# Optimization experiments

Hardware: AMD Instinct MI355X
Metric: run time of the kernel (lower is better)

Reference implementation:

```python
import jax, jax.numpy as jnp
from jax import lax
import numpy as np

# (cin, cout, kernel, pad) for the 18 convs (funs 1,3,5,6,7,9,10,11,13..17,19..23)
CONVS = [(3,32,3,0),(32,64,3,0),(64,128,3,1),(128,64,1,0),(64,128,3,1),
         (128,256,3,1),(256,128,1,0),(128,256,3,0),(256,512,3,1),(512,256,1,0),
         (256,512,3,1),(512,256,1,0),(256,512,3,0),(512,256,3,1),(256,128,1,0),
         (128,64,3,1),(64,32,1,0),(32,6,3,1)]
# maxpool(2,2) after conv index (1-based) -> pool padding (torch pads with -inf, floor mode)
POOL_AFTER = {1: 1, 2: 1, 5: 0, 8: 1, 13: 1}
GT = (0.567, 0.469, 0.206, 0.53)  # hardcoded ground-truth box (cx, cy, w, h), normalized


def _backbone(x, ws, bs):
    for i, (w, b) in enumerate(zip(ws, bs), 1):
        pad = CONVS[i - 1][3]
        x = lax.conv_general_dilated(
            x, w, (1, 1), [(pad, pad), (pad, pad)],
            dimension_numbers=("NCHW", "OIHW", "NCHW")) + b[None, :, None, None]
        if i in POOL_AFTER:
            p = POOL_AFTER[i]
            x = lax.reduce_window(
                x, -jnp.inf, lax.max, (1, 1, 2, 2), (1, 1, 2, 2),
                [(0, 0), (0, 0), (p, p), (p, p)])
    return x


def _head(x):
    # torch: x.transpose(1,3) on [B,6,H,W] -> [B,W,H,6]; j indexes W, k indexes H
    xt = jnp.transpose(x, (0, 3, 2, 1))
    B, W, H, _ = xt.shape
    j = jnp.arange(W, dtype=xt.dtype)[None, :, None]  # [1,W,1]
    k = jnp.arange(H, dtype=xt.dtype)[None, None, :]  # [1,1,H]
    px = (j + xt[..., 2]) / W
    py = (k + xt[..., 3]) / H
    pw = jnp.exp(xt[..., 4]) / W
    ph = jnp.exp(xt[..., 5]) / H
    # center-format IoU against the single gt box (detached mask, as in torch via float())
    iw = jnp.clip(jnp.minimum(px + pw * 0.5, GT[0] + GT[2] * 0.5)
                  - jnp.maximum(px - pw * 0.5, GT[0] - GT[2] * 0.5), 0.0)
    ih = jnp.clip(jnp.minimum(py + ph * 0.5, GT[1] + GT[3] * 0.5)
                  - jnp.maximum(py - ph * 0.5, GT[1] - GT[3] * 0.5), 0.0)
    inter = iw * ih
    iou = inter / (pw * ph + GT[2] * GT[3] - inter)
    iou = lax.stop_gradient(iou)
    tx = GT[0] * W - j          # [1,W,1]
    ty = GT[1] * H - k          # [1,1,H]
    tw = np.log(GT[2] * W).astype(np.float32)
    th = np.log(GT[3] * H).astype(np.float32)
    l1 = (jnp.abs(tx - xt[..., 2]) + jnp.abs(ty - xt[..., 3])
          + jnp.abs(tw - xt[..., 4]) + jnp.abs(th - xt[..., 5]))
    loss = jnp.sum(jnp.where(iou > 0.5, l1, 0.0)).reshape(1)
    return xt, loss


def setup_inputs() -> dict:
    key = jax.random.key(0)
    keys = jax.random.split(key, 1 + 2 * len(CONVS))
    d = {"x": jax.random.normal(keys[0], (16, 3, 416, 416), jnp.float32)}
    for i, (cin, cout, ks, _) in enumerate(CONVS, 1):
        fan_in = cin * ks * ks
        d[f"w{i}"] = jax.random.normal(keys[2 * i - 1], (cout, cin, ks, ks), jnp.float32) / np.sqrt(fan_in)
        d[f"b{i}"] = jax.random.normal(keys[2 * i], (cout,), jnp.float32) * 0.01
    return d


def reference(x, w1, b1, w2, b2, w3, b3, w4, b4, w5, b5, w6, b6, w7, b7, w8, b8,
              w9, b9, w10, b10, w11, b11, w12, b12, w13, b13, w14, b14, w15, b15,
              w16, b16, w17, b17, w18, b18):
    ws = [w1, w2, w3, w4, w5, w6, w7, w8, w9, w10, w11, w12, w13, w14, w15, w16, w17, w18]
    bs = [b1, b2, b3, b4, b5, b6, b7, b8, b9, b10, b11, b12, b13, b14, b15, b16, b17, b18]
    feat = _backbone(x, ws, bs)
    xt, loss = _head(feat)
    return (xt, loss)
```

## Files before the change

### kernel.cpp

```cpp
#include <hip/hip_runtime.h>
#include <math.h>

typedef short v8s __attribute__((ext_vector_type(8)));
typedef float v4f __attribute__((ext_vector_type(4)));

template<int K, int COT, bool POOL>
__global__ __launch_bounds__(256) void conv_fused(
    const float* __restrict__ in, const float* __restrict__ wgt,
    const float* __restrict__ bias, float* __restrict__ out,
    int B, int Cin, int Hin, int Win,
    int Hc, int Wc, int Hout, int Wout,
    int Cout, int cpad, int ppad)
{
    constexpr int NPY = POOL ? 2 : 1;
    constexpr int PS  = K + NPY - 1;
    const int spatial = Hout * Wout;
    const int idx = blockIdx.x * blockDim.x + threadIdx.x;
    const int total = B * spatial;
    if (idx >= total) return;
    const int b  = idx / spatial;
    const int sp = idx - b * spatial;
    const int oy = sp / Wout;
    const int ox = sp - oy * Wout;
    const int co0 = blockIdx.y * COT;

    const int cy0 = POOL ? (2 * oy - ppad) : oy;
    const int cx0 = POOL ? (2 * ox - ppad) : ox;
    const int iy0 = cy0 - cpad;
    const int ix0 = cx0 - cpad;

    bool my[PS], mx[PS];
#pragma unroll
    for (int i = 0; i < PS; i++) {
        my[i] = (unsigned)(iy0 + i) < (unsigned)Hin;
        mx[i] = (unsigned)(ix0 + i) < (unsigned)Win;
    }

    float acc[COT][NPY * NPY];
#pragma unroll
    for (int c = 0; c < COT; c++)
#pragma unroll
        for (int p = 0; p < NPY * NPY; p++) acc[c][p] = 0.f;

    const long inBase = (long)b * Cin * Hin * Win;
    const long wBase  = (long)co0 * Cin * K * K;

    for (int ci = 0; ci < Cin; ci++) {
        const float* ip = in + inBase + (long)ci * Hin * Win;
        float patch[PS][PS];
#pragma unroll
        for (int py = 0; py < PS; py++) {
#pragma unroll
            for (int px = 0; px < PS; px++) {
                float v = 0.f;
                if (my[py] && mx[px]) v = ip[(iy0 + py) * Win + (ix0 + px)];
                patch[py][px] = v;
            }
        }
        const float* wp = wgt + wBase + (long)ci * K * K;
#pragma unroll
        for (int c = 0; c < COT; c++) {
#pragma unroll
            for (int kh = 0; kh < K; kh++)
#pragma unroll
            for (int kw = 0; kw < K; kw++) {
                const float wv = wp[(long)c * Cin * K * K + kh * K + kw];
#pragma unroll
                for (int dy = 0; dy < NPY; dy++)
#pragma unroll
                for (int dx = 0; dx < NPY; dx++)
                    acc[c][dy * NPY + dx] = fmaf(wv, patch[dy + kh][dx + kw],
                                                 acc[c][dy * NPY + dx]);
            }
        }
    }

#pragma unroll
    for (int c = 0; c < COT; c++) {
        float v;
        if (POOL) {
            v = -INFINITY;
#pragma unroll
            for (int dy = 0; dy < NPY; dy++)
#pragma unroll
            for (int dx = 0; dx < NPY; dx++) {
                const int cy = cy0 + dy, cx = cx0 + dx;
                if ((unsigned)cy < (unsigned)Hc && (unsigned)cx < (unsigned)Wc)
                    v = fmaxf(v, acc[c][dy * NPY + dx]);
            }
        } else {
            v = acc[c][0];
        }
        v += bias[co0 + c];
        out[((long)(b * Cout + co0 + c)) * spatial + sp] = v;
    }
}

__device__ __forceinline__ unsigned short f2bf_rne(float x) {
    unsigned u = __float_as_uint(x);
    return (unsigned short)((u + 0x7fffu + ((u >> 16) & 1u)) >> 16);
}
__device__ __forceinline__ float bf2f(unsigned short h) {
    return __uint_as_float(((unsigned)h) << 16);
}

__global__ __launch_bounds__(256) void prepack(
    const float* __restrict__ w, unsigned short* __restrict__ hi,
    unsigned short* __restrict__ lo, int cout, int kdim, int nkb)
{
    int t = blockIdx.x * 256 + threadIdx.x;
    if (t >= cout * kdim) return;
    int co = t / kdim, k = t - co * kdim;
    int cb = co >> 4, m = co & 15, kb = k >> 5, kk = k & 31;
    int lane = ((kk >> 3) << 4) | m, j = kk & 7;
    long dst = ((long)(cb * nkb + kb) << 9) + lane * 8 + j;
    float x = w[t];
    unsigned short h = f2bf_rne(x);
    hi[dst] = h;
    lo[dst] = f2bf_rne(x - bf2f(h));
}

template<int MT, int KS, bool SPLIT>
__global__ __launch_bounds__(256) void conv_mfma(
    const float* __restrict__ in, const unsigned short* __restrict__ whi,
    const unsigned short* __restrict__ wlo, const float* __restrict__ bias,
    float* __restrict__ out, int Cin, int Hin, int Win, int Hc, int Wc,
    int Cout, int pad, int b0, int nb, int nkbTot, int nkbPer, int Mpad)
{
    const int HW = Hc * Wc;
    const int M = nb * HW;
    const int tid = threadIdx.x;
    const int lane = tid & 63;
    const int wv = tid >> 6;
    const int spBase = blockIdx.x * 64;
    const int HWin = Hin * Win;
    const int kb0 = SPLIT ? blockIdx.z * nkbPer : 0;
    const int kb1 = SPLIT ? kb0 + nkbPer : nkbTot;

    __shared__ unsigned short P[2][5120];

    const int spoL = lane >> 2;
    int kkc[2];
    kkc[0] = (tid & 3) + 4 * wv;
    kkc[1] = kkc[0] + 16;

    const float* sptr[4];
    int soy[4], sox[4], soff[4];
    bool sval[4];
#pragma unroll
    for (int j = 0; j < 4; ++j) {
        int spo = spoL + 16 * j;
        int sp = spBase + spo;
        sval[j] = sp < M;
        int q = sval[j] ? sp : 0;
        int b = q / HW; int r = q - b * HW;
        soy[j] = r / Wc; sox[j] = r - soy[j] * Wc;
        soff[j] = soy[j] * Win + sox[j];
        sptr[j] = in + (size_t)(b0 + b) * Cin * HWin;
    }

    int ci[2], r9[2], dh[2], dw[2], koff[2];
#pragma unroll
    for (int m = 0; m < 2; ++m) {
        int k = kb0 * 32 + kkc[m];
        if (KS == 3) {
            ci[m] = k / 9; r9[m] = k - 9 * ci[m];
            int d3 = (r9[m] >= 3) + (r9[m] >= 6);
            dh[m] = d3 - pad; dw[m] = r9[m] - 3 * d3 - pad;
        } else { ci[m] = k; dh[m] = 0; dw[m] = 0; }
        koff[m] = ci[m] * HWin + dh[m] * Win + dw[m];
    }

    float rv[8];
#define STAGE()                                                                \
    {                                                                          \
        _Pragma("unroll")                                                      \
        for (int m = 0; m < 2; ++m)                                            \
        _Pragma("unroll")                                                      \
        for (int j = 0; j < 4; ++j) {                                          \
            int iy = soy[j] + dh[m], ix = sox[j] + dw[m];                      \
            bool ok = sval[j] && ((unsigned)iy < (unsigned)Hin) &&             \
                      ((unsigned)ix < (unsigned)Win);                          \
            rv[m * 4 + j] = ok ? sptr[j][koff[m] + soff[j]] : 0.f;             \
        }                                                                      \
    }
#define ADVANCE()                                                              \
    {                                                                          \
        _Pragma("unroll")                                                      \
        for (int m = 0; m < 2; ++m) {                                          \
            if (KS == 3) {                                                     \
                r9[m] += 5; int c = r9[m] >= 9; r9[m] -= c ? 9 : 0;            \
                ci[m] += 3 + c;                                                \
                int d3 = (r9[m] >= 3) + (r9[m] >= 6);                          \
                dh[m] = d3 - pad; dw[m] = r9[m] - 3 * d3 - pad;                \
                koff[m] = ci[m] * HWin + dh[m] * Win + dw[m];                  \
            } else { koff[m] += 32 * HWin; }                                   \
        }                                                                      \
    }

    STAGE();

    const int g0 = blockIdx.y * (MT * 4) + wv * MT;
    const unsigned short* whp[MT];
    const unsigned short* wlp[MT];
#pragma unroll
    for (int mt = 0; mt < MT; ++mt) {
        size_t base = (((size_t)(g0 + mt) * nkbTot + kb0) << 9) + lane * 8;
        whp[mt] = whi + base; wlp[mt] = wlo + base;
    }

    v4f acc[MT][4];
    {
        v4f z = {0.f, 0.f, 0.f, 0.f};
#pragma unroll
        for (int mt = 0; mt < MT; ++mt)
#pragma unroll
            for (int nt = 0; nt < 4; ++nt) acc[mt][nt] = z;
    }

    for (int kb = kb0; kb < kb1; ++kb) {
        unsigned short* Ph = P[kb & 1];
#pragma unroll
        for (int m = 0; m < 2; ++m)
#pragma unroll
        for (int j = 0; j < 4; ++j) {
            float v = rv[m * 4 + j];
            unsigned vb = __float_as_uint(v);
            float res = v - __uint_as_float(vb & 0xffff0000u);
            int a = (spoL + 16 * j) * 40 + kkc[m];
            Ph[a] = (unsigned short)(vb >> 16);
            Ph[2560 + a] = (unsigned short)(__float_as_uint(res) >> 16);
        }
        __syncthreads();

        v8s wh[MT], wl[MT];
#pragma unroll
        for (int mt = 0; mt < MT; ++mt) {
            wh[mt] = *(const v8s*)whp[mt];
            wl[mt] = *(const v8s*)wlp[mt];
            whp[mt] += 512; wlp[mt] += 512;
        }

        if (kb + 1 < kb1) { ADVANCE(); STAGE(); }

#pragma unroll
        for (int nt = 0; nt < 4; ++nt) {
            int ro = (nt * 16 + (lane & 15)) * 40 + (lane >> 4) * 8;
            v8s ph = *(const v8s*)(Ph + ro);
            v8s pl = *(const v8s*)(Ph + 2560 + ro);
#pragma unroll
            for (int mt = 0; mt < MT; ++mt) {
                acc[mt][nt] = __builtin_amdgcn_mfma_f32_16x16x32_bf16(wh[mt], ph, acc[mt][nt], 0, 0, 0);
                acc[mt][nt] = __builtin_amdgcn_mfma_f32_16x16x32_bf16(wh[mt], pl, acc[mt][nt], 0, 0, 0);
                acc[mt][nt] = __builtin_amdgcn_mfma_f32_16x16x32_bf16(wl[mt], ph, acc[mt][nt], 0, 0, 0);
            }
        }
    }
#undef STAGE
#undef ADVANCE

    const int qrow = (lane >> 4) * 4;
    if (SPLIT) {
        float* pz = out + (size_t)blockIdx.z * Cout * Mpad;
#pragma unroll
        for (int mt = 0; mt < MT; ++mt) {
            int co = (g0 + mt) * 16 + qrow;
#pragma unroll
            for (int nt = 0; nt < 4; ++nt) {
                int sp = spBase + nt * 16 + (lane & 15);
                if (sp < M) {
#pragma unroll
                    for (int r = 0; r < 4; ++r)
                        pz[(size_t)(co + r) * Mpad + sp] = acc[mt][nt][r];
                }
            }
        }
    } else {
#pragma unroll
        for (int mt = 0; mt < MT; ++mt) {
            int co = (g0 + mt) * 16 + qrow;
            float bsv[4];
#pragma unroll
            for (int r = 0; r < 4; ++r) bsv[r] = bias[co + r];
#pragma unroll
            for (int nt = 0; nt < 4; ++nt) {
                int sp = spBase + nt * 16 + (lane & 15);
                if (sp < M) {
                    int b = sp / HW, rsp = sp - b * HW;
                    float* op = out + ((size_t)(b * Cout + co)) * HW + rsp;
#pragma unroll
                    for (int r = 0; r < 4; ++r)
                        op[(size_t)r * HW] = acc[mt][nt][r] + bsv[r];
                }
            }
        }
    }
}

__global__ __launch_bounds__(256) void sk_reduce(
    const float* __restrict__ part, const float* __restrict__ bias,
    float* __restrict__ out, int Cout, int HW, int M, int Mpad, int SK)
{
    int t = blockIdx.x * 256 + threadIdx.x;
    if (t >= Cout * M) return;
    int co = t / M, m = t - co * M;
    float s = bias[co];
    for (int k = 0; k < SK; ++k)
        s += part[((size_t)k * Cout + co) * Mpad + m];
    int b = m / HW, rsp = m - b * HW;
    out[((size_t)(b * Cout + co)) * HW + rsp] = s;
}

__global__ __launch_bounds__(256) void maxpool_k(
    const float* __restrict__ in, float* __restrict__ out,
    int C, int Hc, int Wc, int Hp, int Wp, int p, int total)
{
    int t = blockIdx.x * 256 + threadIdx.x;
    if (t >= total) return;
    int wp2 = Hp * Wp;
    int bc = t / wp2; int r = t - bc * wp2;
    int y = r / Wp, xx = r - y * Wp;
    int y0 = 2 * y - p, x0 = 2 * xx - p;
    const float* ip = in + (size_t)bc * Hc * Wc;
    float v = -INFINITY;
#pragma unroll
    for (int dy = 0; dy < 2; ++dy)
#pragma unroll
    for (int dx = 0; dx < 2; ++dx) {
        int yy = y0 + dy, xc = x0 + dx;
        if ((unsigned)yy < (unsigned)Hc && (unsigned)xc < (unsigned)Wc)
            v = fmaxf(v, ip[yy * Wc + xc]);
    }
    out[t] = v;
}

__global__ __launch_bounds__(1024) void head_kernel(
    const float* __restrict__ x, float* __restrict__ out, int B)
{
    const int W = 13, H = 13;
    const float gx = 0.567f, gy = 0.469f, gw = 0.206f, gh = 0.53f;
    const int tid = threadIdx.x;
    const int total = B * W * H;
    float lsum = 0.f;
    for (int i = tid; i < total; i += blockDim.x) {
        const int b = i / (W * H);
        const int r = i - b * W * H;
        const int j = r / H;
        const int k = r - j * H;
        float v[6];
#pragma unroll
        for (int c = 0; c < 6; c++) {
            v[c] = x[((b * 6 + c) * H + k) * W + j];
            out[((b * W + j) * H + k) * 6 + c] = v[c];
        }
        const float px = (j + v[2]) / (float)W;
        const float py = (k + v[3]) / (float)H;
        const float pw = expf(v[4]) / (float)W;
        const float ph = expf(v[5]) / (float)H;
        float iw = fminf(px + pw * 0.5f, gx + gw * 0.5f)
                 - fmaxf(px - pw * 0.5f, gx - gw * 0.5f);
        iw = fmaxf(iw, 0.f);
        float ih = fminf(py + ph * 0.5f, gy + gh * 0.5f)
                 - fmaxf(py - ph * 0.5f, gy - gh * 0.5f);
        ih = fmaxf(ih, 0.f);
        const float inter = iw * ih;
        const float iou = inter / (pw * ph + gw * gh - inter);
        const float tx = gx * W - (float)j;
        const float ty = gy * H - (float)k;
        const float tw = logf(gw * W);
        const float th = logf(gh * H);
        const float l1 = fabsf(tx - v[2]) + fabsf(ty - v[3])
                       + fabsf(tw - v[4]) + fabsf(th - v[5]);
        if (iou > 0.5f) lsum += l1;
    }
    __shared__ float red[1024];
    red[tid] = lsum;
    __syncthreads();
    for (int s = blockDim.x / 2; s > 0; s >>= 1) {
        if (tid < s) red[tid] += red[tid + s];
        __syncthreads();
    }
    if (tid == 0) out[total * 6] = red[0];
}

extern "C" void kernel_launch(void* const* d_in, const int* in_sizes, int n_in,
                              void* d_out, int out_size, void* d_ws, size_t ws_size,
                              hipStream_t stream)
{
    (void)in_sizes; (void)n_in; (void)out_size;
    const float* x = (const float*)d_in[0];
    const int B = 16;
    const size_t MB = 1024 * 1024;
    char* ws = (char*)d_ws;
    float* bufA = (float*)ws;
    float* bufB = (float*)(ws + 90 * MB);
    unsigned short* WHI = (unsigned short*)(ws + 135 * MB);
    unsigned short* WLO = (unsigned short*)(ws + 147 * MB);
    char* TEMP = ws + 159 * MB;
    const bool gemmOK = ws_size >= 159 * MB;
    const size_t tempAvail = ws_size > 159 * MB ? ws_size - 159 * MB : 0;

    static const struct { int cin, cout, ks, cpad, pool, ppad; } L[18] = {
        {3,  32, 3, 0, 1, 1}, {32, 64, 3, 0, 1, 1}, {64, 128, 3, 1, 0, 0},
        {128, 64, 1, 0, 0, 0}, {64, 128, 3, 1, 1, 0}, {128, 256, 3, 1, 0, 0},
        {256, 128, 1, 0, 0, 0}, {128, 256, 3, 0, 1, 1}, {256, 512, 3, 1, 0, 0},
        {512, 256, 1, 0, 0, 0}, {256, 512, 3, 1, 0, 0}, {512, 256, 1, 0, 0, 0},
        {256, 512, 3, 0, 1, 1}, {512, 256, 3, 1, 0, 0}, {256, 128, 1, 0, 0, 0},
        {128, 64, 3, 1, 0, 0}, {64, 32, 1, 0, 0, 0}, {32, 6, 3, 1, 0, 0}
    };

    if (gemmOK) {
        size_t off = 0;
        for (int i = 1; i <= 15; ++i) {
            int kdim = L[i].cin * L[i].ks * L[i].ks;
            int n = L[i].cout * kdim;
            prepack<<<(n + 255) / 256, 256, 0, stream>>>(
                (const float*)d_in[2 * i + 1], WHI + off, WLO + off,
                L[i].cout, kdim, kdim / 32);
            off += (size_t)n;
        }
    }

    const float* cur = x;
    int Hin = 416, Win = 416;
    size_t woff = 0;

    for (int i = 0; i < 18; ++i) {
        const auto& l = L[i];
        const int Hc = Hin + 2 * l.cpad - l.ks + 1;
        const int Wc = Win + 2 * l.cpad - l.ks + 1;
        const int Hout = l.pool ? (Hc + 2 * l.ppad - 2) / 2 + 1 : Hc;
        const int Wout = l.pool ? (Wc + 2 * l.ppad - 2) / 2 + 1 : Wc;
        float* dst = (i % 2 == 0) ? bufA : bufB;
        const float* w  = (const float*)d_in[2 * i + 1];
        const float* bb = (const float*)d_in[2 * i + 2];
        const int kdim = l.cin * l.ks * l.ks;
        const int nkb = kdim / 32;

        int nb = 16;
        if (l.pool) {
            size_t perImg = (size_t)l.cout * Hc * Wc * 4;
            while (nb && perImg * (size_t)nb > tempAvail) nb >>= 1;
        }
        const bool useG = gemmOK && i >= 1 && i <= 15 && (!l.pool || nb >= 1);

        if (useG) {
            for (int b0 = 0; b0 < B; b0 += nb) {
                const int M = nb * Hc * Wc;
                const int gx = (M + 63) / 64;
                int MTv = (l.cout >= 256 && (long)gx * (l.cout / 256) >= 512) ? 4
                        : (l.cout >= 128 && (long)gx * (l.cout / 128) >= 512) ? 2 : 1;
                int gy = l.cout / (MTv * 64);
                int SK = 1;
                if (!l.pool && (long)gx * gy < 512) {
                    if (nkb % 4 == 0 && (size_t)4 * l.cout * gx * 64 * 4 <= tempAvail) SK = 4;
                    else if (nkb % 2 == 0 && (size_t)2 * l.cout * gx * 64 * 4 <= tempAvail) SK = 2;
                }
                const int nkbPer = nkb / SK;
                const int Mpad = gx * 64;
                float* gout = l.pool ? (float*)TEMP
                            : (SK > 1 ? (float*)TEMP : dst);
                dim3 gr(gx, gy, SK);
#define GL(MTC, KSC, SPL)                                                      \
                conv_mfma<MTC, KSC, SPL><<<gr, 256, 0, stream>>>(              \
                    cur, WHI + woff, WLO + woff, bb, gout, l.cin, Hin, Win,    \
                    Hc, Wc, l.cout, l.cpad, b0, nb, nkb, nkbPer, Mpad)
#define G2(MTC, KSC) do { if (SK > 1) GL(MTC, KSC, true); else GL(MTC, KSC, false); } while (0)
                if (MTv == 4)      { if (l.ks == 3) G2(4, 3); else G2(4, 1); }
                else if (MTv == 2) { if (l.ks == 3) G2(2, 3); else G2(2, 1); }
                else               { if (l.ks == 3) G2(1, 3); else G2(1, 1); }
#undef G2
#undef GL
                if (SK > 1) {
                    int tot = l.cout * M;
                    sk_reduce<<<(tot + 255) / 256, 256, 0, stream>>>(
                        (const float*)TEMP, bb, dst, l.cout, Hc * Wc, M, Mpad, SK);
                }
                if (l.pool) {
                    int total = nb * l.cout * Hout * Wout;
                    maxpool_k<<<(total + 255) / 256, 256, 0, stream>>>(
                        (const float*)TEMP,
                        dst + (size_t)b0 * l.cout * Hout * Wout,
                        l.cout, Hc, Wc, Hout, Wout, l.ppad, total);
                }
            }
        } else {
            const int spatial = Hout * Wout;
#define FLAUNCH(KK, CC, PP)                                                    \
            conv_fused<KK, CC, PP><<<dim3((B * spatial + 255) / 256,           \
                                          l.cout / CC), 256, 0, stream>>>(     \
                cur, w, bb, dst, B, l.cin, Hin, Win, Hc, Wc, Hout, Wout,       \
                l.cout, l.cpad, l.ppad)
            if (l.pool)                           FLAUNCH(3, 4, true);
            else if (l.ks == 3 && l.cout == 6)    FLAUNCH(3, 6, false);
            else if (l.ks == 3)                   FLAUNCH(3, 8, false);
            else                                  FLAUNCH(1, 8, false);
#undef FLAUNCH
        }

        if (i >= 1 && i <= 15) woff += (size_t)l.cout * kdim;
        cur = dst;
        Hin = Hout;
        Win = Wout;
    }

    head_kernel<<<1, 1024, 0, stream>>>(cur, (float*)d_out, B);
}
```

Baseline: 1.544 ms.

## Store activations with a zero halo ring to drop conv bounds checks

Activation buffers get a one-pixel zero border around every plane. A small ring_zero kernel writes the borders, and the MFMA im2col loads, the direct convs, split-K reduce and maxpool all index into the padded layout, so the per-element bounds checks in the gather are gone. The first layer also switches to a COT=8 fused conv with a swapped grid so channel groups sharing the same input tile run together. The cost is extra ring-zeroing launches, larger workspace offsets and padded strides that may misalign accesses. Padded buffers that are read with pad=0 must never depend on the ring being zero.

```diff
diff --git a/kernel.cpp b/kernel.cpp
--- a/kernel.cpp
+++ b/kernel.cpp
@@ -4,25 +4,27 @@
 typedef short v8s __attribute__((ext_vector_type(8)));
 typedef float v4f __attribute__((ext_vector_type(4)));
 
-template<int K, int COT, bool POOL>
+template<int K, int COT, bool POOL, bool MASK, bool SWAP>
 __global__ __launch_bounds__(256) void conv_fused(
     const float* __restrict__ in, const float* __restrict__ wgt,
     const float* __restrict__ bias, float* __restrict__ out,
     int B, int Cin, int Hin, int Win,
     int Hc, int Wc, int Hout, int Wout,
-    int Cout, int cpad, int ppad)
+    int Cout, int cpad, int ppad,
+    int inPS, int inRS, int inOfs, int outPS, int outRS, int outOfs)
 {
     constexpr int NPY = POOL ? 2 : 1;
     constexpr int PS  = K + NPY - 1;
     const int spatial = Hout * Wout;
-    const int idx = blockIdx.x * blockDim.x + threadIdx.x;
+    const int idx = (SWAP ? blockIdx.y : blockIdx.x) * blockDim.x + threadIdx.x;
+    const int cog = SWAP ? blockIdx.x : blockIdx.y;
     const int total = B * spatial;
     if (idx >= total) return;
     const int b  = idx / spatial;
     const int sp = idx - b * spatial;
     const int oy = sp / Wout;
     const int ox = sp - oy * Wout;
-    const int co0 = blockIdx.y * COT;
+    const int co0 = cog * COT;
 
     const int cy0 = POOL ? (2 * oy - ppad) : oy;
     const int cx0 = POOL ? (2 * ox - ppad) : ox;
@@ -32,8 +34,8 @@
     bool my[PS], mx[PS];
 #pragma unroll
     for (int i = 0; i < PS; i++) {
-        my[i] = (unsigned)(iy0 + i) < (unsigned)Hin;
-        mx[i] = (unsigned)(ix0 + i) < (unsigned)Win;
+        my[i] = !MASK || ((unsigned)(iy0 + i) < (unsigned)Hin);
+        mx[i] = !MASK || ((unsigned)(ix0 + i) < (unsigned)Win);
     }
 
     float acc[COT][NPY * NPY];
@@ -42,18 +44,18 @@
 #pragma unroll
         for (int p = 0; p < NPY * NPY; p++) acc[c][p] = 0.f;
 
-    const long inBase = (long)b * Cin * Hin * Win;
+    const float* inB = in + inOfs + (size_t)b * Cin * inPS;
     const long wBase  = (long)co0 * Cin * K * K;
 
     for (int ci = 0; ci < Cin; ci++) {
-        const float* ip = in + inBase + (long)ci * Hin * Win;
+        const float* ip = inB + (size_t)ci * inPS;
         float patch[PS][PS];
 #pragma unroll
         for (int py = 0; py < PS; py++) {
 #pragma unroll
             for (int px = 0; px < PS; px++) {
                 float v = 0.f;
-                if (my[py] && mx[px]) v = ip[(iy0 + py) * Win + (ix0 + px)];
+                if (my[py] && mx[px]) v = ip[(iy0 + py) * inRS + (ix0 + px)];
                 patch[py][px] = v;
             }
         }
@@ -92,8 +94,24 @@
             v = acc[c][0];
         }
         v += bias[co0 + c];
-        out[((long)(b * Cout + co0 + c)) * spatial + sp] = v;
-    }
+        out[outOfs + (size_t)(b * Cout + co0 + c) * outPS + oy * outRS + ox] = v;
+    }
+}
+
+__global__ __launch_bounds__(256) void ring_zero(
+    float* __restrict__ buf, int planes, int H, int W)
+{
+    int Wp = W + 2, Hp = H + 2;
+    int ringlen = 2 * Wp + 2 * H;
+    int t = blockIdx.x * 256 + threadIdx.x;
+    if (t >= planes * ringlen) return;
+    int p = t / ringlen, r = t - p * ringlen;
+    float* pl = buf + (size_t)p * Hp * Wp;
+    int idx;
+    if (r < Wp) idx = r;
+    else if (r < 2 * Wp) idx = (Hp - 1) * Wp + (r - Wp);
+    else { int rr = r - 2 * Wp; int row = 1 + (rr >> 1); idx = row * Wp + ((rr & 1) ? (Wp - 1) : 0); }
+    pl[idx] = 0.f;
 }
 
 __device__ __forceinline__ unsigned short f2bf_rne(float x) {
@@ -124,8 +142,9 @@
 __global__ __launch_bounds__(256) void conv_mfma(
     const float* __restrict__ in, const unsigned short* __restrict__ whi,
     const unsigned short* __restrict__ wlo, const float* __restrict__ bias,
-    float* __restrict__ out, int Cin, int Hin, int Win, int Hc, int Wc,
-    int Cout, int pad, int b0, int nb, int nkbTot, int nkbPer, int Mpad)
+    float* __restrict__ out, int Cin, int inHWp, int inWp, int Hc, int Wc,
+    int Cout, int pad, int b0, int nb, int nkbTot, int nkbPer, int Mpad,
+    int outHWp, int outWp)
 {
     const int HW = Hc * Wc;
     const int M = nb * HW;
@@ -133,7 +152,6 @@
     const int lane = tid & 63;
     const int wv = tid >> 6;
     const int spBase = blockIdx.x * 64;
-    const int HWin = Hin * Win;
     const int kb0 = SPLIT ? blockIdx.z * nkbPer : 0;
     const int kb1 = SPLIT ? kb0 + nkbPer : nkbTot;
 
@@ -145,30 +163,26 @@
     kkc[1] = kkc[0] + 16;
 
     const float* sptr[4];
-    int soy[4], sox[4], soff[4];
-    bool sval[4];
+    int soff[4];
 #pragma unroll
     for (int j = 0; j < 4; ++j) {
-        int spo = spoL + 16 * j;
-        int sp = spBase + spo;
-        sval[j] = sp < M;
-        int q = sval[j] ? sp : 0;
+        int sp = spBase + spoL + 16 * j;
+        int q = sp < M ? sp : M - 1;
         int b = q / HW; int r = q - b * HW;
-        soy[j] = r / Wc; sox[j] = r - soy[j] * Wc;
-        soff[j] = soy[j] * Win + sox[j];
-        sptr[j] = in + (size_t)(b0 + b) * Cin * HWin;
-    }
-
-    int ci[2], r9[2], dh[2], dw[2], koff[2];
+        int soy = r / Wc, sox = r - soy * Wc;
+        soff[j] = (soy + 1) * inWp + (sox + 1);
+        sptr[j] = in + (size_t)(b0 + b) * Cin * inHWp;
+    }
+
+    int ci[2], r9[2], koff[2];
 #pragma unroll
     for (int m = 0; m < 2; ++m) {
         int k = kb0 * 32 + kkc[m];
         if (KS == 3) {
             ci[m] = k / 9; r9[m] = k - 9 * ci[m];
             int d3 = (r9[m] >= 3) + (r9[m] >= 6);
-            dh[m] = d3 - pad; dw[m] = r9[m] - 3 * d3 - pad;
-        } else { ci[m] = k; dh[m] = 0; dw[m] = 0; }
-        koff[m] = ci[m] * HWin + dh[m] * Win + dw[m];
+            koff[m] = ci[m] * inHWp + (d3 - pad) * inWp + (r9[m] - 3 * d3 - pad);
+        } else { ci[m] = k; koff[m] = k * inHWp; }
     }
 
     float rv[8];
@@ -177,12 +191,8 @@
         _Pragma("unroll")                                                      \
         for (int m = 0; m < 2; ++m)                                            \
         _Pragma("unroll")                                                      \
-        for (int j = 0; j < 4; ++j) {                                          \
-            int iy = soy[j] + dh[m], ix = sox[j] + dw[m];                      \
-            bool ok = sval[j] && ((unsigned)iy < (unsigned)Hin) &&             \
-                      ((unsigned)ix < (unsigned)Win);                          \
-            rv[m * 4 + j] = ok ? sptr[j][koff[m] + soff[j]] : 0.f;             \
-        }                                                                      \
+        for (int j = 0; j < 4; ++j)                                            \
+            rv[m * 4 + j] = sptr[j][koff[m] + soff[j]];                        \
     }
 #define ADVANCE()                                                              \
     {                                                                          \
@@ -192,9 +202,9 @@
                 r9[m] += 5; int c = r9[m] >= 9; r9[m] -= c ? 9 : 0;            \
                 ci[m] += 3 + c;                                                \
                 int d3 = (r9[m] >= 3) + (r9[m] >= 6);                          \
-                dh[m] = d3 - pad; dw[m] = r9[m] - 3 * d3 - pad;                \
-                koff[m] = ci[m] * HWin + dh[m] * Win + dw[m];                  \
-            } else { koff[m] += 32 * HWin; }                                   \
+                koff[m] = ci[m] * inHWp + (d3 - pad) * inWp                    \
+                        + (r9[m] - 3 * d3 - pad);                              \
+            } else { koff[m] += 32 * inHWp; }                                  \
         }                                                                      \
     }
 
@@ -287,10 +297,12 @@
                 int sp = spBase + nt * 16 + (lane & 15);
                 if (sp < M) {
                     int b = sp / HW, rsp = sp - b * HW;
-                    float* op = out + ((size_t)(b * Cout + co)) * HW + rsp;
+                    int y = rsp / Wc, xx = rsp - y * Wc;
+                    float* op = out + (size_t)(b * Cout + co) * outHWp
+                              + (size_t)(y + 1) * outWp + (xx + 1);
 #pragma unroll
                     for (int r = 0; r < 4; ++r)
-                        op[(size_t)r * HW] = acc[mt][nt][r] + bsv[r];
+                        op[(size_t)r * outHWp] = acc[mt][nt][r] + bsv[r];
                 }
             }
         }
@@ -299,7 +311,8 @@
 
 __global__ __launch_bounds__(256) void sk_reduce(
     const float* __restrict__ part, const float* __restrict__ bias,
-    float* __restrict__ out, int Cout, int HW, int M, int Mpad, int SK)
+    float* __restrict__ out, int Cout, int HW, int Wc, int M, int Mpad, int SK,
+    int outHWp, int outWp)
 {
     int t = blockIdx.x * 256 + threadIdx.x;
     if (t >= Cout * M) return;
@@ -308,12 +321,14 @@
     for (int k = 0; k < SK; ++k)
         s += part[((size_t)k * Cout + co) * Mpad + m];
     int b = m / HW, rsp = m - b * HW;
-    out[((size_t)(b * Cout + co)) * HW + rsp] = s;
+    int y = rsp / Wc, xx = rsp - y * Wc;
+    out[(size_t)(b * Cout + co) * outHWp + (size_t)(y + 1) * outWp + (xx + 1)] = s;
 }
 
 __global__ __launch_bounds__(256) void maxpool_k(
     const float* __restrict__ in, float* __restrict__ out,
-    int C, int Hc, int Wc, int Hp, int Wp, int p, int total)
+    int Hc, int Wc, int Hp, int Wp, int p, int total,
+    int inHWp, int inWp, int outHWp, int outWp)
 {
     int t = blockIdx.x * 256 + threadIdx.x;
     if (t >= total) return;
@@ -321,7 +336,7 @@
     int bc = t / wp2; int r = t - bc * wp2;
     int y = r / Wp, xx = r - y * Wp;
     int y0 = 2 * y - p, x0 = 2 * xx - p;
-    const float* ip = in + (size_t)bc * Hc * Wc;
+    const float* ip = in + (size_t)bc * inHWp;
     float v = -INFINITY;
 #pragma unroll
     for (int dy = 0; dy < 2; ++dy)
@@ -329,9 +344,9 @@
     for (int dx = 0; dx < 2; ++dx) {
         int yy = y0 + dy, xc = x0 + dx;
         if ((unsigned)yy < (unsigned)Hc && (unsigned)xc < (unsigned)Wc)
-            v = fmaxf(v, ip[yy * Wc + xc]);
-    }
-    out[t] = v;
+            v = fmaxf(v, ip[(yy + 1) * inWp + (xc + 1)]);
+    }
+    out[(size_t)bc * outHWp + (size_t)(y + 1) * outWp + (xx + 1)] = v;
 }
 
 __global__ __launch_bounds__(1024) void head_kernel(
@@ -393,12 +408,12 @@
     const size_t MB = 1024 * 1024;
     char* ws = (char*)d_ws;
     float* bufA = (float*)ws;
-    float* bufB = (float*)(ws + 90 * MB);
-    unsigned short* WHI = (unsigned short*)(ws + 135 * MB);
-    unsigned short* WLO = (unsigned short*)(ws + 147 * MB);
-    char* TEMP = ws + 159 * MB;
-    const bool gemmOK = ws_size >= 159 * MB;
-    const size_t tempAvail = ws_size > 159 * MB ? ws_size - 159 * MB : 0;
+    float* bufB = (float*)(ws + 93 * MB);
+    unsigned short* WHI = (unsigned short*)(ws + 141 * MB);
+    unsigned short* WLO = (unsigned short*)(ws + 153 * MB);
+    char* TEMP = ws + 165 * MB;
+    const bool gemmOK = ws_size >= 166 * MB;
+    const size_t tempAvail = ws_size > 165 * MB ? ws_size - 165 * MB : 0;
 
     static const struct { int cin, cout, ks, cpad, pool, ppad; } L[18] = {
         {3,  32, 3, 0, 1, 1}, {32, 64, 3, 0, 1, 1}, {64, 128, 3, 1, 0, 0},
@@ -408,6 +423,7 @@
         {256, 512, 3, 0, 1, 1}, {512, 256, 3, 1, 0, 0}, {256, 128, 1, 0, 0, 0},
         {128, 64, 3, 1, 0, 0}, {64, 32, 1, 0, 0, 0}, {32, 6, 3, 1, 0, 0}
     };
+    static const bool RING[18] = {0,1,0,1,1,0,0,1,0,1,0,0,1,0,1,0,1,0};
 
     if (gemmOK) {
         size_t off = 0;
@@ -437,9 +453,25 @@
         const int kdim = l.cin * l.ks * l.ks;
         const int nkb = kdim / 32;
 
+        const int inRS  = (i == 0) ? Win : (Win + 2);
+        const int inPS  = (i == 0) ? Hin * Win : (Hin + 2) * (Win + 2);
+        const int inOfs = (i == 0) ? 0 : (inRS + 1);
+        const bool outPad = (i != 17);
+        const int outRS  = outPad ? (Wout + 2) : Wout;
+        const int outPS  = outPad ? (Hout + 2) * (Wout + 2) : Hout * Wout;
+        const int outOfs = outPad ? (outRS + 1) : 0;
+        const int tRS = Wc + 2, tPS = (Hc + 2) * (Wc + 2);
+
+        if (RING[i]) {
+            int planes = B * l.cout;
+            int ringlen = 2 * (Wout + 2) + 2 * Hout;
+            ring_zero<<<(planes * ringlen + 255) / 256, 256, 0, stream>>>(
+                dst, planes, Hout, Wout);
+        }
+
         int nb = 16;
         if (l.pool) {
-            size_t perImg = (size_t)l.cout * Hc * Wc * 4;
+            size_t perImg = (size_t)l.cout * tPS * 4;
             while (nb && perImg * (size_t)nb > tempAvail) nb >>= 1;
         }
         const bool useG = gemmOK && i >= 1 && i <= 15 && (!l.pool || nb >= 1);
@@ -458,13 +490,15 @@
                 }
                 const int nkbPer = nkb / SK;
                 const int Mpad = gx * 64;
-                float* gout = l.pool ? (float*)TEMP
-                            : (SK > 1 ? (float*)TEMP : dst);
+                float* gout = l.pool ? (float*)TEMP : (SK > 1 ? (float*)TEMP : dst);
+                const int gHWp = l.pool ? tPS : (SK > 1 ? 0 : outPS);
+                const int gWp  = l.pool ? tRS : (SK > 1 ? 0 : outRS);
                 dim3 gr(gx, gy, SK);
 #define GL(MTC, KSC, SPL)                                                      \
                 conv_mfma<MTC, KSC, SPL><<<gr, 256, 0, stream>>>(              \
-                    cur, WHI + woff, WLO + woff, bb, gout, l.cin, Hin, Win,    \
-                    Hc, Wc, l.cout, l.cpad, b0, nb, nkb, nkbPer, Mpad)
+                    cur, WHI + woff, WLO + woff, bb, gout, l.cin, inPS, inRS,  \
+                    Hc, Wc, l.cout, l.cpad, b0, nb, nkb, nkbPer, Mpad,         \
+                    gHWp, gWp)
 #define G2(MTC, KSC) do { if (SK > 1) GL(MTC, KSC, true); else GL(MTC, KSC, false); } while (0)
                 if (MTv == 4)      { if (l.ks == 3) G2(4, 3); else G2(4, 1); }
                 else if (MTv == 2) { if (l.ks == 3) G2(2, 3); else G2(2, 1); }
@@ -474,28 +508,33 @@
                 if (SK > 1) {
                     int tot = l.cout * M;
                     sk_reduce<<<(tot + 255) / 256, 256, 0, stream>>>(
-                        (const float*)TEMP, bb, dst, l.cout, Hc * Wc, M, Mpad, SK);
+                        (const float*)TEMP, bb, dst, l.cout, Hc * Wc, Wc, M,
+                        Mpad, SK, outPS, outRS);
                 }
                 if (l.pool) {
                     int total = nb * l.cout * Hout * Wout;
                     maxpool_k<<<(total + 255) / 256, 256, 0, stream>>>(
                         (const float*)TEMP,
-                        dst + (size_t)b0 * l.cout * Hout * Wout,
-                        l.cout, Hc, Wc, Hout, Wout, l.ppad, total);
+                        dst + (size_t)b0 * l.cout * outPS,
+                        Hc, Wc, Hout, Wout, l.ppad, total, tPS, tRS, outPS, outRS);
                 }
             }
         } else {
             const int spatial = Hout * Wout;
-#define FLAUNCH(KK, CC, PP)                                                    \
-            conv_fused<KK, CC, PP><<<dim3((B * spatial + 255) / 256,           \
-                                          l.cout / CC), 256, 0, stream>>>(     \
+#define FL(KK, CC, PP, MM, SW)                                                 \
+            conv_fused<KK, CC, PP, MM, SW><<<                                  \
+                SW ? dim3(l.cout / CC, (B * spatial + 255) / 256)              \
+                   : dim3((B * spatial + 255) / 256, l.cout / CC),             \
+                256, 0, stream>>>(                                             \
                 cur, w, bb, dst, B, l.cin, Hin, Win, Hc, Wc, Hout, Wout,       \
-                l.cout, l.cpad, l.ppad)
-            if (l.pool)                           FLAUNCH(3, 4, true);
-            else if (l.ks == 3 && l.cout == 6)    FLAUNCH(3, 6, false);
-            else if (l.ks == 3)                   FLAUNCH(3, 8, false);
-            else                                  FLAUNCH(1, 8, false);
-#undef FLAUNCH
+                l.cout, l.cpad, l.ppad, inPS, inRS, inOfs, outPS, outRS, outOfs)
+            if (i == 0)                           FL(3, 8, true, true, true);
+            else if (i == 16)                     FL(1, 8, false, false, false);
+            else if (i == 17)                     FL(3, 6, false, false, false);
+            else if (l.pool)                      FL(3, 4, true, true, false);
+            else if (l.ks == 3)                   FL(3, 8, false, true, false);
+            else                                  FL(1, 8, false, true, false);
+#undef FL
         }
 
         if (i >= 1 && i <= 15) woff += (size_t)l.cout * kdim;
```

Result: no change. 1.520 ms (-1.6%).
